# Performance work log

Measured on AMD Instinct MI355X. Metric: run time of the kernel, lower is better.

Reference implementation:

```python
import jax, jax.numpy as jnp
from jax import lax
import numpy as np

HEADS = 4
BUCKET = 64
DEPTH = 4


def _conv(x, w, b):
    y = lax.conv_general_dilated(x, w, (1, 1), [(1, 1), (1, 1)],
                                 dimension_numbers=('NCHW', 'OIHW', 'NCHW'))
    return y + b[None, :, None, None]


def _convT(x, w, b):
    # torch ConvTranspose2d(k=4, s=2, p=1): flip kernel, swap io, lhs_dilation=2, pad k-1-p=2
    wk = jnp.flip(w, (2, 3)).transpose(1, 0, 2, 3)
    y = lax.conv_general_dilated(x, wk, (1, 1), [(2, 2), (2, 2)], lhs_dilation=(2, 2),
                                 dimension_numbers=('NCHW', 'OIHW', 'NCHW'))
    return y + b[None, :, None, None]


def _maxpool(x):
    return lax.reduce_window(x, -jnp.inf, lax.max, (1, 1, 2, 2), (1, 1, 2, 2), 'VALID')


def _ln(x, g, b):
    m = x.mean(-1, keepdims=True)
    v = ((x - m) ** 2).mean(-1, keepdims=True)
    return (x - m) / jnp.sqrt(v + 1e-5) * g + b


def _lsh_attention(x, Wqk, bqk, Wv, bv, Wo, bo, rot):
    # shared-QK LSH bucketed attention (single hash round), look-one-back chunks
    B, N, D = x.shape
    h, dh = HEADS, D // HEADS
    qk = (x @ Wqk + bqk).reshape(B, N, h, dh).transpose(0, 2, 1, 3)  # B h N dh
    v = (x @ Wv + bv).reshape(B, N, h, dh).transpose(0, 2, 1, 3)
    k = qk / (jnp.linalg.norm(qk, axis=-1, keepdims=True) + 1e-6)    # keys = normalized queries
    rotated = jnp.einsum('bhnd,hdr->bhnr', qk, rot)
    buckets = jnp.argmax(jnp.concatenate([rotated, -rotated], -1), -1)  # B h N
    ticker = jnp.arange(N)
    perm = jnp.argsort(buckets * N + ticker, axis=-1)  # stable sort by bucket
    inv_perm = jnp.argsort(perm, axis=-1)
    g = lambda t: jnp.take_along_axis(t, perm[..., None], axis=2)
    nc = N // BUCKET
    bq = g(qk).reshape(B, h, nc, BUCKET, dh)
    bk = g(k).reshape(B, h, nc, BUCKET, dh)
    bv_ = g(v).reshape(B, h, nc, BUCKET, dh)
    bk2 = jnp.concatenate([bk, jnp.roll(bk, 1, axis=2)], axis=3)   # look one chunk back
    bv2 = jnp.concatenate([bv_, jnp.roll(bv_, 1, axis=2)], axis=3)
    dots = jnp.einsum('bhcid,bhcjd->bhcij', bq, bk2) * (dh ** -0.5)
    spos = jnp.take_along_axis(jnp.broadcast_to(ticker, buckets.shape), perm, -1).reshape(B, h, nc, BUCKET)
    kpos = jnp.concatenate([spos, jnp.roll(spos, 1, axis=2)], axis=3)
    dots = jnp.where(spos[..., :, None] == kpos[..., None, :], -1e5, dots)  # mask self (q == k)
    attn = jax.nn.softmax(dots, -1)
    o = jnp.einsum('bhcij,bhcjd->bhcid', attn, bv2).reshape(B, h, N, dh)
    o = jnp.take_along_axis(o, inv_perm[..., None], axis=2)  # unsort
    return o.transpose(0, 2, 1, 3).reshape(B, N, D) @ Wo + bo


def _reformer(seq, ln1_g, ln1_b, Wqk, bqk, Wv, bv, Wo, bo, rot, ln2_g, ln2_b, Wff1, bff1, Wff2, bff2):
    for i in range(DEPTH):
        seq = seq + _lsh_attention(_ln(seq, ln1_g[i], ln1_b[i]), Wqk[i], bqk[i], Wv[i], bv[i], Wo[i], bo[i], rot[i])
        hdn = jax.nn.gelu(_ln(seq, ln2_g[i], ln2_b[i]) @ Wff1[i] + bff1[i])
        seq = seq + hdn @ Wff2[i] + bff2[i]
    return seq


def _forward(burst, conv1_w, conv1_b, conv2_w, conv2_b, conv3_w, conv3_b,
             ln1_g, ln1_b, Wqk, bqk, Wv, bv, Wo, bo, rot, ln2_g, ln2_b,
             Wff1, bff1, Wff2, bff2, up1_w, up1_b, dec1_w, dec1_b,
             up2_w, up2_b, dec2_w, dec2_b, out_w, out_b):
    B, T, C, H, W = burst.shape
    x = burst.reshape(B * T, C, H, W)
    e1 = jax.nn.relu(_conv(x, conv1_w, conv1_b))
    p1 = _maxpool(e1)
    e2 = jax.nn.relu(_conv(p1, conv2_w, conv2_b))
    p2 = _maxpool(e2)
    bm = jax.nn.relu(_conv(p2, conv3_w, conv3_b))
    D = bm.shape[1]
    Hq, Wq = H // 4, W // 4
    seq = bm.transpose(0, 2, 3, 1).reshape(B * T, Hq * Wq, D)
    seq = _reformer(seq, ln1_g, ln1_b, Wqk, bqk, Wv, bv, Wo, bo, rot, ln2_g, ln2_b, Wff1, bff1, Wff2, bff2)
    bm = seq.reshape(B * T, Hq, Wq, D).transpose(0, 3, 1, 2)
    d1 = _convT(bm, up1_w, up1_b)
    d1 = jax.nn.relu(_conv(jnp.concatenate([d1, e2], 1), dec1_w, dec1_b))
    d2 = _convT(d1, up2_w, up2_b)
    d2 = jax.nn.relu(_conv(jnp.concatenate([d2, e1], 1), dec2_w, dec2_b))
    sharp = jax.nn.sigmoid(_conv(d2, out_w, out_b))
    return sharp.reshape(B, T, C, H, W)[:, 0]


def setup_inputs() -> dict:
    key = jax.random.key(0)
    ks = jax.random.split(key, 20)
    s = 0.05
    n = lambda k, shape: jax.random.normal(k, shape, jnp.float32) * s
    inp = {}
    inp['burst'] = jax.random.uniform(ks[0], (1, 7, 3, 256, 256), jnp.float32)
    inp['conv1_w'] = n(ks[1], (64, 3, 3, 3)); inp['conv1_b'] = jnp.zeros((64,), jnp.float32)
    inp['conv2_w'] = n(ks[2], (128, 64, 3, 3)); inp['conv2_b'] = jnp.zeros((128,), jnp.float32)
    inp['conv3_w'] = n(ks[3], (256, 128, 3, 3)); inp['conv3_b'] = jnp.zeros((256,), jnp.float32)
    inp['ln1_g'] = jnp.ones((4, 256), jnp.float32); inp['ln1_b'] = jnp.zeros((4, 256), jnp.float32)
    inp['Wqk'] = n(ks[4], (4, 256, 256)); inp['bqk'] = jnp.zeros((4, 256), jnp.float32)
    inp['Wv'] = n(ks[5], (4, 256, 256)); inp['bv'] = jnp.zeros((4, 256), jnp.float32)
    inp['Wo'] = n(ks[6], (4, 256, 256)); inp['bo'] = jnp.zeros((4, 256), jnp.float32)
    inp['rot'] = jax.random.normal(ks[7], (4, 4, 64, 32), jnp.float32)  # depth, heads, d_head, n_buckets//2
    inp['ln2_g'] = jnp.ones((4, 256), jnp.float32); inp['ln2_b'] = jnp.zeros((4, 256), jnp.float32)
    inp['Wff1'] = n(ks[8], (4, 256, 1024)); inp['bff1'] = jnp.zeros((4, 1024), jnp.float32)
    inp['Wff2'] = n(ks[9], (4, 1024, 256)); inp['bff2'] = jnp.zeros((4, 256), jnp.float32)
    inp['up1_w'] = n(ks[10], (256, 128, 4, 4)); inp['up1_b'] = jnp.zeros((128,), jnp.float32)
    inp['dec1_w'] = n(ks[11], (128, 256, 3, 3)); inp['dec1_b'] = jnp.zeros((128,), jnp.float32)
    inp['up2_w'] = n(ks[12], (128, 64, 4, 4)); inp['up2_b'] = jnp.zeros((64,), jnp.float32)
    inp['dec2_w'] = n(ks[13], (64, 128, 3, 3)); inp['dec2_b'] = jnp.zeros((64,), jnp.float32)
    inp['out_w'] = n(ks[14], (3, 64, 3, 3)); inp['out_b'] = jnp.zeros((3,), jnp.float32)
    return inp


def reference(burst, conv1_w, conv1_b, conv2_w, conv2_b, conv3_w, conv3_b,
              ln1_g, ln1_b, Wqk, bqk, Wv, bv, Wo, bo, rot, ln2_g, ln2_b,
              Wff1, bff1, Wff2, bff2, up1_w, up1_b, dec1_w, dec1_b,
              up2_w, up2_b, dec2_w, dec2_b, out_w, out_b):
    return _forward(burst, conv1_w, conv1_b, conv2_w, conv2_b, conv3_w, conv3_b,
                    ln1_g, ln1_b, Wqk, bqk, Wv, bv, Wo, bo, rot, ln2_g, ln2_b,
                    Wff1, bff1, Wff2, bff2, up1_w, up1_b, dec1_w, dec1_b,
                    up2_w, up2_b, dec2_w, dec2_b, out_w, out_b)
```

## Files before the change

kernel.cpp:

```cpp
#include <hip/hip_runtime.h>
#include <hip/hip_bf16.h>
#include <math.h>

using short8  = __attribute__((ext_vector_type(8))) short;
using half8   = __attribute__((ext_vector_type(8))) _Float16;
using floatx4 = __attribute__((ext_vector_type(4))) float;

static __device__ __forceinline__ float gelu_f(float x) {
    float x3 = x * x * x;
    return 0.5f * x * (1.f + tanhf(0.7978845608028654f * (x + 0.044715f * x3)));
}

static __device__ __forceinline__ short f2h(float f) {
    _Float16 h = (_Float16)f;
    return __builtin_bit_cast(short, h);
}


template <int OCB>
__global__ __launch_bounds__(256) void conv3x3_kernel(
    const float* __restrict__ in1, int C1, const float* __restrict__ in2, int C2,
    const float* __restrict__ w, const float* __restrict__ bias,
    float* __restrict__ out, int H, int W, int OC, int act, int nhwc_out)
{
    int tx = threadIdx.x, ty = threadIdx.y;
    int x = blockIdx.x * 16 + tx, y = blockIdx.y * 16 + ty;
    int oc0 = blockIdx.z * OCB;
    int C = C1 + C2;
    float acc[OCB];
#pragma unroll
    for (int o = 0; o < OCB; ++o) acc[o] = 0.f;
    for (int ic = 0; ic < C; ++ic) {
        const float* src = (ic < C1) ? (in1 + (size_t)ic * H * W)
                                     : (in2 + (size_t)(ic - C1) * H * W);
        float v[9];
#pragma unroll
        for (int ky = 0; ky < 3; ++ky) {
            int iy = y + ky - 1;
            bool okY = (iy >= 0) && (iy < H);
#pragma unroll
            for (int kx = 0; kx < 3; ++kx) {
                int ix = x + kx - 1;
                bool ok = okY && (ix >= 0) && (ix < W);
                v[ky * 3 + kx] = ok ? src[(size_t)iy * W + ix] : 0.f;
            }
        }
        const float* wp = w + ((size_t)oc0 * C + ic) * 9;
#pragma unroll
        for (int o = 0; o < OCB; ++o) {
            const float* wo = wp + (size_t)o * C * 9;
            acc[o] += v[0]*wo[0] + v[1]*wo[1] + v[2]*wo[2]
                    + v[3]*wo[3] + v[4]*wo[4] + v[5]*wo[5]
                    + v[6]*wo[6] + v[7]*wo[7] + v[8]*wo[8];
        }
    }
#pragma unroll
    for (int o = 0; o < OCB; ++o) {
        int oc = oc0 + o;
        float r = acc[o] + bias[oc];
        if (act == 1) r = fmaxf(r, 0.f);
        else if (act == 2) r = 1.f / (1.f + expf(-r));
        if (nhwc_out) out[(size_t)(y * W + x) * OC + oc] = r;
        else          out[(size_t)oc * H * W + (size_t)y * W + x] = r;
    }
}

__global__ __launch_bounds__(256) void conv3x3_lds_kernel(
    const float* __restrict__ in, const float* __restrict__ w,
    const float* __restrict__ bias, float* __restrict__ out,
    int H, int W, int C, int OC, int nhwc_out)
{
    __shared__ float s[16 * 324];
    int tid = threadIdx.x;
    int tx = tid & 15, ty = tid >> 4;
    int x0 = blockIdx.x * 16, y0 = blockIdx.y * 16;
    int oc0 = blockIdx.z * 8;
    int HW = H * W;
    float acc[8];
#pragma unroll
    for (int o = 0; o < 8; ++o) acc[o] = 0.f;
    for (int ic0 = 0; ic0 < C; ic0 += 16) {
        __syncthreads();
        for (int idx = tid; idx < 16 * 324; idx += 256) {
            int ic = idx / 324;
            int r = idx - ic * 324;
            int yy = r / 18;
            int xx = r - yy * 18;
            int gy = y0 + yy - 1, gx = x0 + xx - 1;
            float v = 0.f;
            if (gy >= 0 && gy < H && gx >= 0 && gx < W)
                v = in[(size_t)(ic0 + ic) * HW + (size_t)gy * W + gx];
            s[idx] = v;
        }
        __syncthreads();
        for (int ic = 0; ic < 16; ++ic) {
            const float* sc = s + ic * 324;
            float v[9];
            v[0] = sc[(ty + 0) * 18 + tx + 0];
            v[1] = sc[(ty + 0) * 18 + tx + 1];
            v[2] = sc[(ty + 0) * 18 + tx + 2];
            v[3] = sc[(ty + 1) * 18 + tx + 0];
            v[4] = sc[(ty + 1) * 18 + tx + 1];
            v[5] = sc[(ty + 1) * 18 + tx + 2];
            v[6] = sc[(ty + 2) * 18 + tx + 0];
            v[7] = sc[(ty + 2) * 18 + tx + 1];
            v[8] = sc[(ty + 2) * 18 + tx + 2];
            const float* wp = w + ((size_t)oc0 * C + ic0 + ic) * 9;
#pragma unroll
            for (int o = 0; o < 8; ++o) {
                const float* wo = wp + (size_t)o * C * 9;
                acc[o] += v[0]*wo[0] + v[1]*wo[1] + v[2]*wo[2]
                        + v[3]*wo[3] + v[4]*wo[4] + v[5]*wo[5]
                        + v[6]*wo[6] + v[7]*wo[7] + v[8]*wo[8];
            }
        }
    }
    int x = x0 + tx, y = y0 + ty;
#pragma unroll
    for (int o = 0; o < 8; ++o) {
        int oc = oc0 + o;
        float r = fmaxf(acc[o] + bias[oc], 0.f);
        if (nhwc_out) out[(size_t)(y * W + x) * OC + oc] = r;
        else          out[(size_t)oc * HW + (size_t)y * W + x] = r;
    }
}

__global__ __launch_bounds__(256) void maxpool_kernel(
    const float* __restrict__ in, float* __restrict__ out, int C, int IH, int IW)
{
    int OH = IH >> 1, OW = IW >> 1;
    int idx = blockIdx.x * 256 + threadIdx.x;
    int total = C * OH * OW;
    if (idx >= total) return;
    int x = idx % OW; int t = idx / OW; int y = t % OH; int c = t / OH;
    const float* p = in + (size_t)c * IH * IW + (size_t)(2 * y) * IW + 2 * x;
    out[idx] = fmaxf(fmaxf(p[0], p[1]), fmaxf(p[IW], p[IW + 1]));
}

__global__ __launch_bounds__(256) void ln_kernel(
    const float* __restrict__ x, const float* __restrict__ g,
    const float* __restrict__ b, float* __restrict__ y, short* __restrict__ yh)
{
    int wave = threadIdx.x >> 6, lane = threadIdx.x & 63;
    int n = blockIdx.x * 4 + wave;
    const float* xr = x + (size_t)n * 256;
    float4 v = *(const float4*)(xr + lane * 4);
    float s = v.x + v.y + v.z + v.w;
#pragma unroll
    for (int m = 1; m < 64; m <<= 1) s += __shfl_xor(s, m);
    float mean = s * (1.f / 256.f);
    float cx = v.x - mean, cy = v.y - mean, cz = v.z - mean, cw = v.w - mean;
    float q = cx * cx + cy * cy + cz * cz + cw * cw;
#pragma unroll
    for (int m = 1; m < 64; m <<= 1) q += __shfl_xor(q, m);
    float rstd = rsqrtf(q * (1.f / 256.f) + 1e-5f);
    float4 gv = *(const float4*)(g + lane * 4);
    float4 bv = *(const float4*)(b + lane * 4);
    float4 o;
    o.x = cx * rstd * gv.x + bv.x;
    o.y = cy * rstd * gv.y + bv.y;
    o.z = cz * rstd * gv.z + bv.z;
    o.w = cw * rstd * gv.w + bv.w;
    *(float4*)(y + (size_t)n * 256 + lane * 4) = o;
    short* yp = yh + (size_t)n * 256 + lane * 4;
    yp[0] = f2h(o.x); yp[1] = f2h(o.y); yp[2] = f2h(o.z); yp[3] = f2h(o.w);
}

static __device__ __forceinline__ void gemm_core(
    const float* __restrict__ A, const float* __restrict__ W,
    const float* __restrict__ bias, float* __restrict__ Cp,
    int N, int K, int act, int resid, int m0, int n0)
{
    __shared__ float As[16][68];
    __shared__ float Ws[16][68];
    int tid = threadIdx.x;
    int tx = tid & 15, ty = tid >> 4;
    int lm = tid & 63, lk = (tid >> 6) * 4;
    int lwk = tid >> 4, lwn = (tid & 15) * 4;
    const float* Ap = A + (size_t)(m0 + lm) * K + lk;
    const float* Wp = W + (size_t)lwk * N + n0 + lwn;
    float4 av = *(const float4*)Ap;
    float4 wv = *(const float4*)Wp;
    float acc[4][4];
#pragma unroll
    for (int i = 0; i < 4; ++i)
#pragma unroll
        for (int j = 0; j < 4; ++j) acc[i][j] = 0.f;
    for (int k0 = 0; k0 < K; k0 += 16) {
        As[lk + 0][lm] = av.x; As[lk + 1][lm] = av.y;
        As[lk + 2][lm] = av.z; As[lk + 3][lm] = av.w;
        *(float4*)(&Ws[lwk][lwn]) = wv;
        __syncthreads();
        if (k0 + 16 < K) {
            av = *(const float4*)(Ap + k0 + 16);
            wv = *(const float4*)(Wp + (size_t)(k0 + 16) * N);
        }
#pragma unroll
        for (int kk = 0; kk < 16; ++kk) {
            float4 a4 = *(const float4*)(&As[kk][ty * 4]);
            float4 w4 = *(const float4*)(&Ws[kk][tx * 4]);
            acc[0][0] += a4.x * w4.x; acc[0][1] += a4.x * w4.y; acc[0][2] += a4.x * w4.z; acc[0][3] += a4.x * w4.w;
            acc[1][0] += a4.y * w4.x; acc[1][1] += a4.y * w4.y; acc[1][2] += a4.y * w4.z; acc[1][3] += a4.y * w4.w;
            acc[2][0] += a4.z * w4.x; acc[2][1] += a4.z * w4.y; acc[2][2] += a4.z * w4.z; acc[2][3] += a4.z * w4.w;
            acc[3][0] += a4.w * w4.x; acc[3][1] += a4.w * w4.y; acc[3][2] += a4.w * w4.z; acc[3][3] += a4.w * w4.w;
        }
        __syncthreads();
    }
#pragma unroll
    for (int i = 0; i < 4; ++i) {
        int cm = m0 + ty * 4 + i;
#pragma unroll
        for (int j = 0; j < 4; ++j) {
            int cn = n0 + tx * 4 + j;
            float v = acc[i][j] + bias[cn];
            if (act == 1) v = gelu_f(v);
            float* cp = Cp + (size_t)cm * N + cn;
            if (resid) v += *cp;
            *cp = v;
        }
    }
}

__global__ __launch_bounds__(256) void gemm_kernel(
    const float* __restrict__ A, const float* __restrict__ W,
    const float* __restrict__ bias, float* __restrict__ C,
    int M, int N, int K, int act, int resid)
{
    gemm_core(A, W, bias, C, N, K, act, resid, blockIdx.y * 64, blockIdx.x * 64);
}

__global__ __launch_bounds__(256) void gemm_qkv_kernel(
    const float* __restrict__ A,
    const float* __restrict__ W1, const float* __restrict__ b1, float* __restrict__ C1,
    const float* __restrict__ W2, const float* __restrict__ b2, float* __restrict__ C2,
    int K)
{
    int side = blockIdx.x >> 2;
    const float* W = side ? W2 : W1;
    const float* b = side ? b2 : b1;
    float* C = side ? C2 : C1;
    gemm_core(A, W, b, C, 256, K, 0, 0, blockIdx.y * 64, (blockIdx.x & 3) * 64);
}

__global__ __launch_bounds__(256) void knorm_kernel(
    const float* __restrict__ qk, float* __restrict__ knrm)
{
    int t = blockIdx.x * 256 + threadIdx.x;
    int h = t >> 12, n = t & 4095;
    const float* q = qk + (size_t)n * 256 + h * 64;
    float s = 0.f;
#pragma unroll
    for (int d = 0; d < 64; d += 4) {
        float4 v = *(const float4*)(q + d);
        s += v.x * v.x + v.y * v.y + v.z * v.z + v.w * v.w;
    }
    knrm[t] = 1.f / (sqrtf(s) + 1e-6f);
}

__global__ __launch_bounds__(256) void bucket_kernel(
    const float* __restrict__ qk, const float* __restrict__ rot,
    int* __restrict__ buckets)
{
    int t = blockIdx.x * 256 + threadIdx.x;
    int h = t >> 12, n = t & 4095;
    const float* q = qk + (size_t)n * 256 + h * 64;
    const float* R = rot + (size_t)h * 2048;
    float acc[32];
#pragma unroll
    for (int r = 0; r < 32; ++r) acc[r] = 0.f;
    for (int d = 0; d < 64; ++d) {
        float qd = q[d];
        const float* Rd = R + d * 32;
#pragma unroll
        for (int r = 0; r < 32; ++r) acc[r] += qd * Rd[r];
    }
    float bvv = acc[0]; int best = 0;
#pragma unroll
    for (int j = 1; j < 64; ++j) {
        float val = (j < 32) ? acc[j] : -acc[j - 32];
        if (val > bvv) { bvv = val; best = j; }
    }
    buckets[t] = best;
}

__global__ __launch_bounds__(256) void lsh_sort_kernel(
    const int* __restrict__ buckets, int* __restrict__ perm)
{
    int h = blockIdx.x;
    const int* bk = buckets + h * 4096;
    __shared__ unsigned long long mask[64][64];
    __shared__ int counts[64];
    __shared__ int offsets[64];
    __shared__ int wpre[64][64];
    int tid = threadIdx.x, wave = tid >> 6, lane = tid & 63;
    for (int w = wave * 16; w < wave * 16 + 16; ++w) {
        int bl = bk[w * 64 + lane];
        for (int b = 0; b < 64; ++b) {
            unsigned long long m = __ballot(bl == b);
            if (lane == b) mask[b][w] = m;
        }
    }
    __syncthreads();
    if (tid < 64) {
        int c = 0;
        for (int w = 0; w < 64; ++w) c += __popcll(mask[tid][w]);
        counts[tid] = c;
    }
    __syncthreads();
    if (tid == 0) {
        int a = 0;
        for (int b = 0; b < 64; ++b) { offsets[b] = a; a += counts[b]; }
    }
    __syncthreads();
    for (int b = wave * 16; b < wave * 16 + 16; ++b) {
        int c = __popcll(mask[b][lane]);
        int incl = c;
#pragma unroll
        for (int off = 1; off < 64; off <<= 1) {
            int nb = __shfl_up(incl, off);
            if (lane >= off) incl += nb;
        }
        wpre[b][lane] = incl - c + offsets[b];
    }
    __syncthreads();
    for (int i = tid; i < 4096; i += 256) {
        int b = bk[i]; int w = i >> 6; int l = i & 63;
        unsigned long long below = mask[b][w] & ((1ull << l) - 1ull);
        int pos = wpre[b][w] + __popcll(below);
        perm[h * 4096 + pos] = i;
    }
}

__global__ __launch_bounds__(256) void attn_kernel(
    const float* __restrict__ qk, const float* __restrict__ vv,
    const float* __restrict__ knrm, const int* __restrict__ perm,
    float* __restrict__ o, short* __restrict__ oh)
{
    __shared__ float ks[128 * 64];
    __shared__ float dotsT[128 * 64];
    int c = blockIdx.x, h = blockIdx.y;
    int tid = threadIdx.x;
    const int* pm = perm + h * 4096;
    int cm = (c + 63) & 63;
    {
        int jr = tid >> 1, hf = tid & 1;
        int sk = (jr < 64) ? (c * 64 + jr) : (cm * 64 + (jr - 64));
        int nk = pm[sk];
        float sc = knrm[h * 4096 + nk];
        const float* src = qk + (size_t)nk * 256 + h * 64 + hf * 32;
        float* dst = ks + jr * 64 + hf * 32;
#pragma unroll
        for (int d = 0; d < 32; d += 4) {
            float4 v = *(const float4*)(src + d);
            v.x *= sc; v.y *= sc; v.z *= sc; v.w *= sc;
            *(float4*)(dst + d) = v;
        }
    }
    __syncthreads();
    int r = tid & 63, jg = tid >> 6;
    int nq = pm[c * 64 + r];
    {
        float qreg[64];
        const float* src = qk + (size_t)nq * 256 + h * 64;
#pragma unroll
        for (int d = 0; d < 64; d += 4) {
            float4 v = *(const float4*)(src + d);
            qreg[d] = v.x; qreg[d + 1] = v.y; qreg[d + 2] = v.z; qreg[d + 3] = v.w;
        }
        for (int j = jg * 32; j < jg * 32 + 32; ++j) {
            const float* kr = ks + j * 64;
            float dot = 0.f;
#pragma unroll
            for (int d = 0; d < 64; ++d) dot += qreg[d] * kr[d];
            int sk = (j < 64) ? (c * 64 + j) : (cm * 64 + (j - 64));
            int nk = pm[sk];
            dot = (nk == nq) ? -1e5f : dot * 0.125f;
            dotsT[j * 64 + r] = dot;
        }
    }
    __syncthreads();
    {
        int jr = tid >> 1, hf = tid & 1;
        int sk = (jr < 64) ? (c * 64 + jr) : (cm * 64 + (jr - 64));
        int nk = pm[sk];
        const float* src = vv + (size_t)nk * 256 + h * 64 + hf * 32;
        float* dst = ks + jr * 64 + hf * 32;
#pragma unroll
        for (int d = 0; d < 32; d += 4)
            *(float4*)(dst + d) = *(const float4*)(src + d);
    }
    if (tid < 64) {
        int rr = tid;
        float mx = -1e30f;
        for (int j = 0; j < 128; ++j) mx = fmaxf(mx, dotsT[j * 64 + rr]);
        float s = 0.f;
        for (int j = 0; j < 128; ++j) {
            float e = expf(dotsT[j * 64 + rr] - mx);
            dotsT[j * 64 + rr] = e; s += e;
        }
        float inv = 1.f / s;
        for (int j = 0; j < 128; ++j) dotsT[j * 64 + rr] *= inv;
    }
    __syncthreads();
    int dg = jg;
    float acc[16];
#pragma unroll
    for (int d = 0; d < 16; ++d) acc[d] = 0.f;
    for (int j = 0; j < 128; ++j) {
        float a = dotsT[j * 64 + r];
        const float* vr = ks + j * 64 + dg * 16;
#pragma unroll
        for (int d = 0; d < 16; ++d) acc[d] += a * vr[d];
    }
    size_t ob = (size_t)nq * 256 + h * 64 + dg * 16;
    float* dst = o + ob;
    short* dsth = oh + ob;
#pragma unroll
    for (int d = 0; d < 16; d += 4) {
        float4 v = { acc[d], acc[d + 1], acc[d + 2], acc[d + 3] };
        *(float4*)(dst + d) = v;
        dsth[d] = f2h(v.x); dsth[d+1] = f2h(v.y);
        dsth[d+2] = f2h(v.z); dsth[d+3] = f2h(v.w);
    }
}


__global__ void pack_gemm_kernel(const float* __restrict__ W, short* __restrict__ Bp,
                                 int N, int total)
{
    int t = blockIdx.x * 256 + threadIdx.x;
    if (t >= total) return;
    int lane = t & 63, fi = t >> 6;
    int NT = N >> 4;
    int nt = fi % NT, kt = fi / NT;
    int n = nt * 16 + (lane & 15);
    int k0 = kt * 32 + (lane >> 4) * 8;
    short8 v;
#pragma unroll
    for (int j = 0; j < 8; ++j) v[j] = f2h(W[(size_t)(k0 + j) * N + n]);
    ((short8*)Bp)[t] = v;
}

__global__ void pack_conv_kernel(const float* __restrict__ w, short* __restrict__ Bp,
                                 int C, int OC, int NT, int total)
{
    int t = blockIdx.x * 256 + threadIdx.x;
    if (t >= total) return;
    int lane = t & 63, fi = t >> 6;
    int nt = fi % NT, kt = fi / NT;
    int cpt = C >> 5;
    int tap = kt / cpt, ct = kt % cpt;
    int c = ct * 32 + (lane >> 4) * 8;
    int oc = nt * 16 + (lane & 15);
    short8 v;
#pragma unroll
    for (int j = 0; j < 8; ++j) {
        float f = (oc < OC) ? w[((size_t)oc * C + c + j) * 9 + tap] : 0.f;
        v[j] = f2h(f);
    }
    ((short8*)Bp)[t] = v;
}

__global__ void pack_convt_kernel(const float* __restrict__ w, short* __restrict__ Bp,
                                  int IC, int OC, int total)
{
    int t = blockIdx.x * 256 + threadIdx.x;
    if (t >= total) return;
    int lane = t & 63, fi = t >> 6;
    int NT = OC >> 4, cpt = IC >> 5, KT4 = 4 * cpt;
    int nt = fi % NT, r = fi / NT;
    int kt = r % KT4, pz = r / KT4;
    int py = pz >> 1, px = pz & 1;
    int t4 = kt / cpt, ct = kt % cpt;
    int ty = t4 >> 1, tx = t4 & 1;
    int ky = py ? (2 * ty) : (1 + 2 * ty);
    int kx = px ? (2 * tx) : (1 + 2 * tx);
    int ic = ct * 32 + (lane >> 4) * 8;
    int oc = nt * 16 + (lane & 15);
    short8 v;
#pragma unroll
    for (int j = 0; j < 8; ++j)
        v[j] = f2h(w[(((size_t)(ic + j) * OC + oc) * 4 + ky) * 4 + kx]);
    ((short8*)Bp)[t] = v;
}

__global__ __launch_bounds__(256) void gemm_mfma_kernel(
    const short* __restrict__ A, const short* __restrict__ Bp,
    const float* __restrict__ bias, float* __restrict__ Cf, short* __restrict__ Cb,
    int M, int N, int K, int act, int resid)
{
    int tid = threadIdx.x, wave = tid >> 6, lane = tid & 63;
    int quad = lane >> 4, l16 = lane & 15;
    int m0 = blockIdx.y * 64 + wave * 16;
    int NT = N >> 4;
    int nt0 = blockIdx.x * 4;
    const half8* arow = (const half8*)(A + (size_t)(m0 + l16) * K + quad * 8);
    const half8* bp = (const half8*)Bp;
    floatx4 acc0 = {0,0,0,0}, acc1 = {0,0,0,0}, acc2 = {0,0,0,0}, acc3 = {0,0,0,0};
    int KT = K >> 5;
    for (int kt = 0; kt < KT; ++kt) {
        half8 a = arow[kt * 4];
        size_t bi = ((size_t)kt * NT + nt0) * 64 + lane;
        acc0 = __builtin_amdgcn_mfma_f32_16x16x32_f16(a, bp[bi      ], acc0, 0, 0, 0);
        acc1 = __builtin_amdgcn_mfma_f32_16x16x32_f16(a, bp[bi +  64], acc1, 0, 0, 0);
        acc2 = __builtin_amdgcn_mfma_f32_16x16x32_f16(a, bp[bi + 128], acc2, 0, 0, 0);
        acc3 = __builtin_amdgcn_mfma_f32_16x16x32_f16(a, bp[bi + 192], acc3, 0, 0, 0);
    }
    floatx4 accs[4] = {acc0, acc1, acc2, acc3};
#pragma unroll
    for (int s = 0; s < 4; ++s) {
        int n = (nt0 + s) * 16 + l16;
        float bs = bias[n];
#pragma unroll
        for (int r = 0; r < 4; ++r) {
            int m = m0 + quad * 4 + r;
            float v = accs[s][r] + bs;
            if (act == 1) v = gelu_f(v);
            size_t o = (size_t)m * N + n;
            if (resid) v += Cf[o];
            if (Cb) Cb[o] = f2h(v);
            else    Cf[o] = v;
        }
    }
}

__global__ __launch_bounds__(256) void conv_mfma_kernel(
    const short* __restrict__ in1, int C1, const short* __restrict__ in2, int C2,
    const short* __restrict__ Bp, const float* __restrict__ bias,
    float* __restrict__ outf, short* __restrict__ outb, int H, int W, int OC)
{
    int tid = threadIdx.x, wave = tid >> 6, lane = tid & 63;
    int quad = lane >> 4, l16 = lane & 15;
    int x0 = blockIdx.x * 64, y = blockIdx.y, nt0 = blockIdx.z * 4;
    int C = C1 + C2, cpt = C >> 5, NT = OC >> 4;
    const half8* bp = (const half8*)Bp;
    floatx4 acc0 = {0,0,0,0}, acc1 = {0,0,0,0}, acc2 = {0,0,0,0}, acc3 = {0,0,0,0};
    int xm = x0 + wave * 16 + l16;
    for (int ky = 0; ky < 3; ++ky) {
        int yy = y + ky - 1;
        bool rok = (yy >= 0) && (yy < H);
        for (int kx = 0; kx < 3; ++kx) {
            int xx = xm + kx - 1;
            bool ok = rok && (xx >= 0) && (xx < W);
            int pos = yy * W + xx;
            int ktb = (ky * 3 + kx) * cpt;
            for (int ct = 0; ct < cpt; ++ct) {
                int cc = ct * 32 + quad * 8;
                half8 a = {};
                if (ok) {
                    const short* src = (cc < C1) ? (in1 + (size_t)pos * C1 + cc)
                                                 : (in2 + (size_t)pos * C2 + (cc - C1));
                    a = *(const half8*)src;
                }
                size_t bi = ((size_t)(ktb + ct) * NT + nt0) * 64 + lane;
                acc0 = __builtin_amdgcn_mfma_f32_16x16x32_f16(a, bp[bi      ], acc0, 0, 0, 0);
                acc1 = __builtin_amdgcn_mfma_f32_16x16x32_f16(a, bp[bi +  64], acc1, 0, 0, 0);
                acc2 = __builtin_amdgcn_mfma_f32_16x16x32_f16(a, bp[bi + 128], acc2, 0, 0, 0);
                acc3 = __builtin_amdgcn_mfma_f32_16x16x32_f16(a, bp[bi + 192], acc3, 0, 0, 0);
            }
        }
    }
    floatx4 accs[4] = {acc0, acc1, acc2, acc3};
#pragma unroll
    for (int s = 0; s < 4; ++s) {
        int n = (nt0 + s) * 16 + l16;
        float bs = bias[n];
#pragma unroll
        for (int r = 0; r < 4; ++r) {
            int m = wave * 16 + quad * 4 + r;
            int x = x0 + m;
            float v = fmaxf(accs[s][r] + bs, 0.f);
            size_t o = ((size_t)y * W + x) * OC + n;
            if (outb) outb[o] = f2h(v);
            else      outf[o] = v;
        }
    }
}

__global__ __launch_bounds__(256) void convt_mfma_kernel(
    const short* __restrict__ in, int IC, const short* __restrict__ Bp,
    const float* __restrict__ bias, short* __restrict__ outb, int IH, int IW, int OC)
{
    int tid = threadIdx.x, wave = tid >> 6, lane = tid & 63;
    int quad = lane >> 4, l16 = lane & 15;
    int pz = blockIdx.z & 3, nt0 = (blockIdx.z >> 2) * 4;
    int py = pz >> 1, px = pz & 1;
    int a0 = blockIdx.y, b0 = blockIdx.x * 64;
    int cpt = IC >> 5, NT = OC >> 4, KT4 = 4 * cpt;
    const half8* bp = (const half8*)Bp;
    floatx4 acc0 = {0,0,0,0}, acc1 = {0,0,0,0}, acc2 = {0,0,0,0}, acc3 = {0,0,0,0};
    int bm = b0 + wave * 16 + l16;
    for (int ty = 0; ty < 2; ++ty) {
        int iy = a0 + (py ? (1 - ty) : (-ty));
        bool rok = (iy >= 0) && (iy < IH);
        for (int tx = 0; tx < 2; ++tx) {
            int ix = bm + (px ? (1 - tx) : (-tx));
            bool ok = rok && (ix >= 0) && (ix < IW);
            int pos = iy * IW + ix;
            int ktb = (ty * 2 + tx) * cpt;
            for (int ct = 0; ct < cpt; ++ct) {
                int cc = ct * 32 + quad * 8;
                half8 a = {};
                if (ok) a = *(const half8*)(in + (size_t)pos * IC + cc);
                size_t bi = ((size_t)(pz * KT4 + ktb + ct) * NT + nt0) * 64 + lane;
                acc0 = __builtin_amdgcn_mfma_f32_16x16x32_f16(a, bp[bi      ], acc0, 0, 0, 0);
                acc1 = __builtin_amdgcn_mfma_f32_16x16x32_f16(a, bp[bi +  64], acc1, 0, 0, 0);
                acc2 = __builtin_amdgcn_mfma_f32_16x16x32_f16(a, bp[bi + 128], acc2, 0, 0, 0);
                acc3 = __builtin_amdgcn_mfma_f32_16x16x32_f16(a, bp[bi + 192], acc3, 0, 0, 0);
            }
        }
    }
    floatx4 accs[4] = {acc0, acc1, acc2, acc3};
    int OW = IW * 2;
    int oy = 2 * a0 + py;
#pragma unroll
    for (int s = 0; s < 4; ++s) {
        int n = (nt0 + s) * 16 + l16;
        float bs = bias[n];
#pragma unroll
        for (int r = 0; r < 4; ++r) {
            int m = wave * 16 + quad * 4 + r;
            int ox = 2 * (b0 + m) + px;
            float v = accs[s][r] + bs;
            outb[((size_t)oy * OW + ox) * OC + n] = f2h(v);
        }
    }
}

__global__ __launch_bounds__(256) void convout_mfma_kernel(
    const short* __restrict__ in, const short* __restrict__ Bp,
    const float* __restrict__ bias, float* __restrict__ out, int H, int W)
{
    int tid = threadIdx.x, wave = tid >> 6, lane = tid & 63;
    int quad = lane >> 4, l16 = lane & 15;
    int x0 = blockIdx.x * 64, y = blockIdx.y;
    const int C = 64, cpt = 2;
    const half8* bp = (const half8*)Bp;
    floatx4 acc = {0,0,0,0};
    int xm = x0 + wave * 16 + l16;
    for (int ky = 0; ky < 3; ++ky) {
        int yy = y + ky - 1;
        bool rok = (yy >= 0) && (yy < H);
        for (int kx = 0; kx < 3; ++kx) {
            int xx = xm + kx - 1;
            bool ok = rok && (xx >= 0) && (xx < W);
            int pos = yy * W + xx;
            int ktb = (ky * 3 + kx) * cpt;
#pragma unroll
            for (int ct = 0; ct < cpt; ++ct) {
                int cc = ct * 32 + quad * 8;
                half8 a = {};
                if (ok) a = *(const half8*)(in + (size_t)pos * C + cc);
                acc = __builtin_amdgcn_mfma_f32_16x16x32_f16(
                          a, bp[(size_t)(ktb + ct) * 64 + lane], acc, 0, 0, 0);
            }
        }
    }
    int oc = l16;
    if (oc < 3) {
        float bs = bias[oc];
#pragma unroll
        for (int r = 0; r < 4; ++r) {
            int m = wave * 16 + quad * 4 + r;
            int x = x0 + m;
            float v = acc[r] + bs;
            v = 1.f / (1.f + expf(-v));
            out[(size_t)oc * H * W + (size_t)y * W + x] = v;
        }
    }
}

__global__ __launch_bounds__(256) void nchw2nhwc_h_kernel(
    const float* __restrict__ in, short* __restrict__ out, int C, int HW)
{
    __shared__ float t[32][33];
    int c0 = blockIdx.y * 32, p0 = blockIdx.x * 32;
    int tid = threadIdx.x;
#pragma unroll
    for (int it = 0; it < 4; ++it) {
        int i = tid + it * 256;
        int lc = i >> 5, lp = i & 31;
        t[lc][lp] = in[(size_t)(c0 + lc) * HW + p0 + lp];
    }
    __syncthreads();
#pragma unroll
    for (int it = 0; it < 4; ++it) {
        int i = tid + it * 256;
        int lp = i >> 5, lc = i & 31;
        out[(size_t)(p0 + lp) * C + c0 + lc] = f2h(t[lc][lp]);
    }
}

__global__ __launch_bounds__(256) void f2h_kernel(
    const float* __restrict__ in, short* __restrict__ out, int n)
{
    int i = blockIdx.x * 256 + threadIdx.x;
    if (i < n) out[i] = f2h(in[i]);
}

extern "C" void kernel_launch(void* const* d_in, const int* in_sizes, int n_in,
                              void* d_out, int out_size, void* d_ws, size_t ws_size,
                              hipStream_t stream)
{
    const float* burst   = (const float*)d_in[0];
    const float* conv1_w = (const float*)d_in[1];  const float* conv1_b = (const float*)d_in[2];
    const float* conv2_w = (const float*)d_in[3];  const float* conv2_b = (const float*)d_in[4];
    const float* conv3_w = (const float*)d_in[5];  const float* conv3_b = (const float*)d_in[6];
    const float* ln1_g   = (const float*)d_in[7];  const float* ln1_b   = (const float*)d_in[8];
    const float* Wqk     = (const float*)d_in[9];  const float* bqk     = (const float*)d_in[10];
    const float* Wv      = (const float*)d_in[11]; const float* bvv     = (const float*)d_in[12];
    const float* Wo      = (const float*)d_in[13]; const float* bo      = (const float*)d_in[14];
    const float* rot     = (const float*)d_in[15];
    const float* ln2_g   = (const float*)d_in[16]; const float* ln2_b   = (const float*)d_in[17];
    const float* Wff1    = (const float*)d_in[18]; const float* bff1    = (const float*)d_in[19];
    const float* Wff2    = (const float*)d_in[20]; const float* bff2    = (const float*)d_in[21];
    const float* up1_w   = (const float*)d_in[22]; const float* up1_b   = (const float*)d_in[23];
    const float* dec1_w  = (const float*)d_in[24]; const float* dec1_b  = (const float*)d_in[25];
    const float* up2_w   = (const float*)d_in[26]; const float* up2_b   = (const float*)d_in[27];
    const float* dec2_w  = (const float*)d_in[28]; const float* dec2_b  = (const float*)d_in[29];
    const float* out_w   = (const float*)d_in[30]; const float* out_b   = (const float*)d_in[31];

    float* ws = (float*)d_ws;
    float* e1   = ws + 0;
    float* e2   = ws + 4194304;
    float* p1   = ws + 6291456;
    float* p2   = ws + 7340032;
    float* seq  = ws + 7864320;
    float* xn   = ws + 8912896;
    float* qkb  = ws + 9961472;
    float* vvb  = ws + 11010048;
    float* oob  = ws + 12058624;
    float* hdn  = ws + 13107200;
    float* knb  = ws + 17301504;
    int* buckets = (int*)(ws + 17317888);
    int* perm    = (int*)(ws + 17334272);
    short* xnh  = (short*)p1;
    short* seqh = (short*)(ws + 6815744);
    short* ooh  = (short*)p2;
    short* hdnh = (short*)hdn;
    short* e1h  = (short*)(ws + 15204352);
    short* e2h  = (short*)vvb;
    short* d1   = (short*)xn;
    short* d1c  = (short*)qkb;
    short* d2   = (short*)hdn;
    short* d2c  = (short*)e2;
    short* pk    = (short*)(ws + 17350656);
    short* ppo   = pk + 65536;
    short* ppf1  = pk + 131072;
    short* ppf2  = pk + 393216;
    short* pdec1 = pk + 655360;
    short* pdec2 = pk + 950272;
    short* pout  = pk + 1024000;
    short* pup1  = pk + 1033216;
    short* pup2  = pk + 1557504;

    dim3 b16(16, 16);

    pack_gemm_kernel<<<32, 256, 0, stream>>>(Wo  + 3 * 65536,  ppo,  256, 8192);
    pack_gemm_kernel<<<128, 256, 0, stream>>>(Wff1 + 3 * 262144, ppf1, 1024, 32768);
    pack_gemm_kernel<<<128, 256, 0, stream>>>(Wff2 + 3 * 262144, ppf2, 256, 32768);
    pack_conv_kernel<<<144, 256, 0, stream>>>(dec1_w, pdec1, 256, 128, 8, 36864);
    pack_conv_kernel<<<36, 256, 0, stream>>>(dec2_w, pdec2, 128, 64, 4, 9216);
    pack_conv_kernel<<<5, 256, 0, stream>>>(out_w,  pout,  64, 3, 1, 1152);
    pack_convt_kernel<<<256, 256, 0, stream>>>(up1_w, pup1, 256, 128, 65536);
    pack_convt_kernel<<<64, 256, 0, stream>>>(up2_w, pup2, 128, 64, 16384);

    conv3x3_kernel<8><<<dim3(16, 16, 8), b16, 0, stream>>>(
        burst, 3, nullptr, 0, conv1_w, conv1_b, e1, 256, 256, 64, 1, 0);
    maxpool_kernel<<<4096, 256, 0, stream>>>(e1, p1, 64, 256, 256);
    conv3x3_lds_kernel<<<dim3(8, 8, 16), 256, 0, stream>>>(
        p1, conv2_w, conv2_b, e2, 128, 128, 64, 128, 0);
    maxpool_kernel<<<2048, 256, 0, stream>>>(e2, p2, 128, 128, 128);
    conv3x3_lds_kernel<<<dim3(4, 4, 32), 256, 0, stream>>>(
        p2, conv3_w, conv3_b, seq, 64, 64, 128, 256, 1);

    for (int i = 0; i < 3; ++i) {
        ln_kernel<<<1024, 256, 0, stream>>>(seq, ln1_g + i * 256, ln1_b + i * 256, xn, xnh);
        gemm_qkv_kernel<<<dim3(8, 64), 256, 0, stream>>>(
            xn, Wqk + i * 65536, bqk + i * 256, qkb,
            Wv + i * 65536, bvv + i * 256, vvb, 256);
        knorm_kernel<<<64, 256, 0, stream>>>(qkb, knb);
        bucket_kernel<<<64, 256, 0, stream>>>(qkb, rot + i * 8192, buckets);
        lsh_sort_kernel<<<4, 256, 0, stream>>>(buckets, perm);
        attn_kernel<<<dim3(64, 4), 256, 0, stream>>>(qkb, vvb, knb, perm, oob, ooh);
        gemm_kernel<<<dim3(4, 64), 256, 0, stream>>>(oob, Wo + i * 65536, bo + i * 256,
                                                     seq, 4096, 256, 256, 0, 1);
        ln_kernel<<<1024, 256, 0, stream>>>(seq, ln2_g + i * 256, ln2_b + i * 256, xn, xnh);
        gemm_kernel<<<dim3(16, 64), 256, 0, stream>>>(xn, Wff1 + i * 262144, bff1 + i * 1024,
                                                      hdn, 4096, 1024, 256, 1, 0);
        gemm_kernel<<<dim3(4, 64), 256, 0, stream>>>(hdn, Wff2 + i * 262144, bff2 + i * 256,
                                                     seq, 4096, 256, 1024, 0, 1);
    }

    {
        const int i = 3;
        ln_kernel<<<1024, 256, 0, stream>>>(seq, ln1_g + i * 256, ln1_b + i * 256, xn, xnh);
        gemm_qkv_kernel<<<dim3(8, 64), 256, 0, stream>>>(
            xn, Wqk + i * 65536, bqk + i * 256, qkb,
            Wv + i * 65536, bvv + i * 256, vvb, 256);
        knorm_kernel<<<64, 256, 0, stream>>>(qkb, knb);
        bucket_kernel<<<64, 256, 0, stream>>>(qkb, rot + i * 8192, buckets);
        lsh_sort_kernel<<<4, 256, 0, stream>>>(buckets, perm);
        attn_kernel<<<dim3(64, 4), 256, 0, stream>>>(qkb, vvb, knb, perm, oob, ooh);
        gemm_mfma_kernel<<<dim3(4, 64), 256, 0, stream>>>(
            ooh, ppo, bo + i * 256, seq, nullptr, 4096, 256, 256, 0, 1);
        ln_kernel<<<1024, 256, 0, stream>>>(seq, ln2_g + i * 256, ln2_b + i * 256, xn, xnh);
        gemm_mfma_kernel<<<dim3(16, 64), 256, 0, stream>>>(
            xnh, ppf1, bff1 + i * 1024, nullptr, hdnh, 4096, 1024, 256, 1, 0);
        gemm_mfma_kernel<<<dim3(4, 64), 256, 0, stream>>>(
            hdnh, ppf2, bff2 + i * 256, seq, nullptr, 4096, 256, 1024, 0, 1);
    }

    nchw2nhwc_h_kernel<<<dim3(2048, 2), 256, 0, stream>>>(e1, e1h, 64, 65536);
    nchw2nhwc_h_kernel<<<dim3(512, 4), 256, 0, stream>>>(e2, e2h, 128, 16384);
    f2h_kernel<<<4096, 256, 0, stream>>>(seq, seqh, 1048576);

    convt_mfma_kernel<<<dim3(1, 64, 8), 256, 0, stream>>>(
        seqh, 256, pup1, up1_b, d1, 64, 64, 128);
    conv_mfma_kernel<<<dim3(2, 128, 2), 256, 0, stream>>>(
        d1, 128, e2h, 128, pdec1, dec1_b, nullptr, d1c, 128, 128, 128);
    convt_mfma_kernel<<<dim3(2, 128, 4), 256, 0, stream>>>(
        d1c, 128, pup2, up2_b, d2, 128, 128, 64);
    conv_mfma_kernel<<<dim3(4, 256, 1), 256, 0, stream>>>(
        d2, 64, e1h, 64, pdec2, dec2_b, nullptr, d2c, 256, 256, 64);
    convout_mfma_kernel<<<dim3(4, 256), 256, 0, stream>>>(
        d2c, pout, out_b, (float*)d_out, 256, 256);
}
```

Before: 1.431 ms.

## Run all transformer GEMMs on bf16x3 split-precision MFMA instead of fp32 FMA

Replaces the LDS-tiled fp32 SIMT GEMM used for layers 0-2 (and the fp16 MFMA used for layer 3) with a GEMM that splits each fp32 operand into three bf16 parts and does six MFMA products, giving close to fp32 accuracy on matrix cores. Weights are packed per layer into three bf16 planes by a new packing kernel inside the layer loop, and activations are split on the fly. This removes the scalar-FMA cost of the first three layers, but adds per-layer packing launches and six times the MFMA work per tile. It also removes the fp16 side outputs and dead conv parameters as cleanup.

```diff
diff --git a/kernel.cpp b/kernel.cpp
--- a/kernel.cpp
+++ b/kernel.cpp
@@ -10,29 +10,34 @@
     float x3 = x * x * x;
     return 0.5f * x * (1.f + tanhf(0.7978845608028654f * (x + 0.044715f * x3)));
 }
-
 static __device__ __forceinline__ short f2h(float f) {
     _Float16 h = (_Float16)f;
     return __builtin_bit_cast(short, h);
 }
+static __device__ __forceinline__ short f2bf(float f) {
+    unsigned u = __float_as_uint(f);
+    u += 0x7fffu + ((u >> 16) & 1u);
+    return (short)(u >> 16);
+}
+static __device__ __forceinline__ float bf2f(short s) {
+    return __uint_as_float(((unsigned)(unsigned short)s) << 16);
+}
 
 
 template <int OCB>
 __global__ __launch_bounds__(256) void conv3x3_kernel(
-    const float* __restrict__ in1, int C1, const float* __restrict__ in2, int C2,
+    const float* __restrict__ in1, int C,
     const float* __restrict__ w, const float* __restrict__ bias,
-    float* __restrict__ out, int H, int W, int OC, int act, int nhwc_out)
+    float* __restrict__ out, int H, int W, int OC)
 {
     int tx = threadIdx.x, ty = threadIdx.y;
     int x = blockIdx.x * 16 + tx, y = blockIdx.y * 16 + ty;
     int oc0 = blockIdx.z * OCB;
-    int C = C1 + C2;
     float acc[OCB];
 #pragma unroll
     for (int o = 0; o < OCB; ++o) acc[o] = 0.f;
     for (int ic = 0; ic < C; ++ic) {
-        const float* src = (ic < C1) ? (in1 + (size_t)ic * H * W)
-                                     : (in2 + (size_t)(ic - C1) * H * W);
+        const float* src = in1 + (size_t)ic * H * W;
         float v[9];
 #pragma unroll
         for (int ky = 0; ky < 3; ++ky) {
@@ -57,11 +62,7 @@
 #pragma unroll
     for (int o = 0; o < OCB; ++o) {
         int oc = oc0 + o;
-        float r = acc[o] + bias[oc];
-        if (act == 1) r = fmaxf(r, 0.f);
-        else if (act == 2) r = 1.f / (1.f + expf(-r));
-        if (nhwc_out) out[(size_t)(y * W + x) * OC + oc] = r;
-        else          out[(size_t)oc * H * W + (size_t)y * W + x] = r;
+        out[(size_t)oc * H * W + (size_t)y * W + x] = fmaxf(acc[o] + bias[oc], 0.f);
     }
 }
 
@@ -139,7 +140,7 @@
 
 __global__ __launch_bounds__(256) void ln_kernel(
     const float* __restrict__ x, const float* __restrict__ g,
-    const float* __restrict__ b, float* __restrict__ y, short* __restrict__ yh)
+    const float* __restrict__ b, float* __restrict__ y)
 {
     int wave = threadIdx.x >> 6, lane = threadIdx.x & 63;
     int n = blockIdx.x * 4 + wave;
@@ -162,84 +163,6 @@
     o.z = cz * rstd * gv.z + bv.z;
     o.w = cw * rstd * gv.w + bv.w;
     *(float4*)(y + (size_t)n * 256 + lane * 4) = o;
-    short* yp = yh + (size_t)n * 256 + lane * 4;
-    yp[0] = f2h(o.x); yp[1] = f2h(o.y); yp[2] = f2h(o.z); yp[3] = f2h(o.w);
-}
-
-static __device__ __forceinline__ void gemm_core(
-    const float* __restrict__ A, const float* __restrict__ W,
-    const float* __restrict__ bias, float* __restrict__ Cp,
-    int N, int K, int act, int resid, int m0, int n0)
-{
-    __shared__ float As[16][68];
-    __shared__ float Ws[16][68];
-    int tid = threadIdx.x;
-    int tx = tid & 15, ty = tid >> 4;
-    int lm = tid & 63, lk = (tid >> 6) * 4;
-    int lwk = tid >> 4, lwn = (tid & 15) * 4;
-    const float* Ap = A + (size_t)(m0 + lm) * K + lk;
-    const float* Wp = W + (size_t)lwk * N + n0 + lwn;
-    float4 av = *(const float4*)Ap;
-    float4 wv = *(const float4*)Wp;
-    float acc[4][4];
-#pragma unroll
-    for (int i = 0; i < 4; ++i)
-#pragma unroll
-        for (int j = 0; j < 4; ++j) acc[i][j] = 0.f;
-    for (int k0 = 0; k0 < K; k0 += 16) {
-        As[lk + 0][lm] = av.x; As[lk + 1][lm] = av.y;
-        As[lk + 2][lm] = av.z; As[lk + 3][lm] = av.w;
-        *(float4*)(&Ws[lwk][lwn]) = wv;
-        __syncthreads();
-        if (k0 + 16 < K) {
-            av = *(const float4*)(Ap + k0 + 16);
-            wv = *(const float4*)(Wp + (size_t)(k0 + 16) * N);
-        }
-#pragma unroll
-        for (int kk = 0; kk < 16; ++kk) {
-            float4 a4 = *(const float4*)(&As[kk][ty * 4]);
-            float4 w4 = *(const float4*)(&Ws[kk][tx * 4]);
-            acc[0][0] += a4.x * w4.x; acc[0][1] += a4.x * w4.y; acc[0][2] += a4.x * w4.z; acc[0][3] += a4.x * w4.w;
-            acc[1][0] += a4.y * w4.x; acc[1][1] += a4.y * w4.y; acc[1][2] += a4.y * w4.z; acc[1][3] += a4.y * w4.w;
-            acc[2][0] += a4.z * w4.x; acc[2][1] += a4.z * w4.y; acc[2][2] += a4.z * w4.z; acc[2][3] += a4.z * w4.w;
-            acc[3][0] += a4.w * w4.x; acc[3][1] += a4.w * w4.y; acc[3][2] += a4.w * w4.z; acc[3][3] += a4.w * w4.w;
-        }
-        __syncthreads();
-    }
-#pragma unroll
-    for (int i = 0; i < 4; ++i) {
-        int cm = m0 + ty * 4 + i;
-#pragma unroll
-        for (int j = 0; j < 4; ++j) {
-            int cn = n0 + tx * 4 + j;
-            float v = acc[i][j] + bias[cn];
-            if (act == 1) v = gelu_f(v);
-            float* cp = Cp + (size_t)cm * N + cn;
-            if (resid) v += *cp;
-            *cp = v;
-        }
-    }
-}
-
-__global__ __launch_bounds__(256) void gemm_kernel(
-    const float* __restrict__ A, const float* __restrict__ W,
-    const float* __restrict__ bias, float* __restrict__ C,
-    int M, int N, int K, int act, int resid)
-{
-    gemm_core(A, W, bias, C, N, K, act, resid, blockIdx.y * 64, blockIdx.x * 64);
-}
-
-__global__ __launch_bounds__(256) void gemm_qkv_kernel(
-    const float* __restrict__ A,
-    const float* __restrict__ W1, const float* __restrict__ b1, float* __restrict__ C1,
-    const float* __restrict__ W2, const float* __restrict__ b2, float* __restrict__ C2,
-    int K)
-{
-    int side = blockIdx.x >> 2;
-    const float* W = side ? W2 : W1;
-    const float* b = side ? b2 : b1;
-    float* C = side ? C2 : C1;
-    gemm_core(A, W, b, C, 256, K, 0, 0, blockIdx.y * 64, (blockIdx.x & 3) * 64);
 }
 
 __global__ __launch_bounds__(256) void knorm_kernel(
@@ -334,7 +257,7 @@
 __global__ __launch_bounds__(256) void attn_kernel(
     const float* __restrict__ qk, const float* __restrict__ vv,
     const float* __restrict__ knrm, const int* __restrict__ perm,
-    float* __restrict__ o, short* __restrict__ oh)
+    float* __restrict__ o)
 {
     __shared__ float ks[128 * 64];
     __shared__ float dotsT[128 * 64];
@@ -412,21 +335,18 @@
 #pragma unroll
         for (int d = 0; d < 16; ++d) acc[d] += a * vr[d];
     }
-    size_t ob = (size_t)nq * 256 + h * 64 + dg * 16;
-    float* dst = o + ob;
-    short* dsth = oh + ob;
+    float* dst = o + (size_t)nq * 256 + h * 64 + dg * 16;
 #pragma unroll
     for (int d = 0; d < 16; d += 4) {
         float4 v = { acc[d], acc[d + 1], acc[d + 2], acc[d + 3] };
         *(float4*)(dst + d) = v;
-        dsth[d] = f2h(v.x); dsth[d+1] = f2h(v.y);
-        dsth[d+2] = f2h(v.z); dsth[d+3] = f2h(v.w);
-    }
-}
-
-
-__global__ void pack_gemm_kernel(const float* __restrict__ W, short* __restrict__ Bp,
-                                 int N, int total)
+    }
+}
+
+
+__global__ void pack_gemm3_kernel(const float* __restrict__ W,
+                                  short* __restrict__ B0, short* __restrict__ B1,
+                                  short* __restrict__ B2, int N, int total)
 {
     int t = blockIdx.x * 256 + threadIdx.x;
     if (t >= total) return;
@@ -435,10 +355,100 @@
     int nt = fi % NT, kt = fi / NT;
     int n = nt * 16 + (lane & 15);
     int k0 = kt * 32 + (lane >> 4) * 8;
-    short8 v;
-#pragma unroll
-    for (int j = 0; j < 8; ++j) v[j] = f2h(W[(size_t)(k0 + j) * N + n]);
-    ((short8*)Bp)[t] = v;
+    short8 v0, v1, v2;
+#pragma unroll
+    for (int j = 0; j < 8; ++j) {
+        float v = W[(size_t)(k0 + j) * N + n];
+        short c0 = f2bf(v); float r = v - bf2f(c0);
+        short c1 = f2bf(r); r -= bf2f(c1);
+        short c2 = f2bf(r);
+        v0[j] = c0; v1[j] = c1; v2[j] = c2;
+    }
+    ((short8*)B0)[t] = v0;
+    ((short8*)B1)[t] = v1;
+    ((short8*)B2)[t] = v2;
+}
+
+static __device__ __forceinline__ void gemm_bf3_core(
+    const float* __restrict__ A,
+    const short* __restrict__ B0, const short* __restrict__ B1,
+    const short* __restrict__ B2, const float* __restrict__ bias,
+    float* __restrict__ C, int N, int K, int act, int resid, int bx, int by)
+{
+    int tid = threadIdx.x, wave = tid >> 6, lane = tid & 63;
+    int quad = lane >> 4, l16 = lane & 15;
+    int m0 = by * 64 + wave * 16;
+    int NT = N >> 4, nt0 = bx * 4;
+    const float* arow = A + (size_t)(m0 + l16) * K + quad * 8;
+    const short8* b0p = (const short8*)B0;
+    const short8* b1p = (const short8*)B1;
+    const short8* b2p = (const short8*)B2;
+    floatx4 aM[4] = {{0,0,0,0},{0,0,0,0},{0,0,0,0},{0,0,0,0}};
+    floatx4 aC[4] = {{0,0,0,0},{0,0,0,0},{0,0,0,0},{0,0,0,0}};
+    int KT = K >> 5;
+    for (int kt = 0; kt < KT; ++kt) {
+        float4 u0 = *(const float4*)(arow + kt * 32);
+        float4 u1 = *(const float4*)(arow + kt * 32 + 4);
+        float vv[8] = {u0.x, u0.y, u0.z, u0.w, u1.x, u1.y, u1.z, u1.w};
+        short8 A0, A1, A2;
+#pragma unroll
+        for (int j = 0; j < 8; ++j) {
+            float v = vv[j];
+            short c0 = f2bf(v); float r = v - bf2f(c0);
+            short c1 = f2bf(r); r -= bf2f(c1);
+            short c2 = f2bf(r);
+            A0[j] = c0; A1[j] = c1; A2[j] = c2;
+        }
+        size_t bi = ((size_t)kt * NT + nt0) * 64 + lane;
+#pragma unroll
+        for (int s = 0; s < 4; ++s) {
+            short8 w0 = b0p[bi + s * 64];
+            short8 w1 = b1p[bi + s * 64];
+            short8 w2 = b2p[bi + s * 64];
+            aM[s] = __builtin_amdgcn_mfma_f32_16x16x32_bf16(A0, w0, aM[s], 0, 0, 0);
+            aC[s] = __builtin_amdgcn_mfma_f32_16x16x32_bf16(A0, w1, aC[s], 0, 0, 0);
+            aC[s] = __builtin_amdgcn_mfma_f32_16x16x32_bf16(A1, w0, aC[s], 0, 0, 0);
+            aC[s] = __builtin_amdgcn_mfma_f32_16x16x32_bf16(A0, w2, aC[s], 0, 0, 0);
+            aC[s] = __builtin_amdgcn_mfma_f32_16x16x32_bf16(A1, w1, aC[s], 0, 0, 0);
+            aC[s] = __builtin_amdgcn_mfma_f32_16x16x32_bf16(A2, w0, aC[s], 0, 0, 0);
+        }
+    }
+#pragma unroll
+    for (int s = 0; s < 4; ++s) {
+        int n = (nt0 + s) * 16 + l16;
+        float bs = bias[n];
+#pragma unroll
+        for (int r = 0; r < 4; ++r) {
+            int m = m0 + quad * 4 + r;
+            float v = aM[s][r] + aC[s][r] + bs;
+            if (act == 1) v = gelu_f(v);
+            size_t o = (size_t)m * N + n;
+            if (resid) v += C[o];
+            C[o] = v;
+        }
+    }
+}
+
+__global__ __launch_bounds__(256) void gemm_bf3_kernel(
+    const float* __restrict__ A,
+    const short* __restrict__ B0, const short* __restrict__ B1,
+    const short* __restrict__ B2, const float* __restrict__ bias,
+    float* __restrict__ C, int N, int K, int act, int resid)
+{
+    gemm_bf3_core(A, B0, B1, B2, bias, C, N, K, act, resid, blockIdx.x, blockIdx.y);
+}
+
+__global__ __launch_bounds__(256) void gemm_qkv_bf3_kernel(
+    const float* __restrict__ A,
+    const short* __restrict__ Q0, const short* __restrict__ Q1, const short* __restrict__ Q2,
+    const float* __restrict__ qb, float* __restrict__ Cq,
+    const short* __restrict__ V0, const short* __restrict__ V1, const short* __restrict__ V2,
+    const float* __restrict__ vb, float* __restrict__ Cv, int K)
+{
+    int side = blockIdx.x >> 2;
+    gemm_bf3_core(A, side ? V0 : Q0, side ? V1 : Q1, side ? V2 : Q2,
+                  side ? vb : qb, side ? Cv : Cq, 256, K, 0, 0,
+                  blockIdx.x & 3, blockIdx.y);
 }
 
 __global__ void pack_conv_kernel(const float* __restrict__ w, short* __restrict__ Bp,
@@ -484,57 +494,17 @@
     ((short8*)Bp)[t] = v;
 }
 
-__global__ __launch_bounds__(256) void gemm_mfma_kernel(
-    const short* __restrict__ A, const short* __restrict__ Bp,
-    const float* __restrict__ bias, float* __restrict__ Cf, short* __restrict__ Cb,
-    int M, int N, int K, int act, int resid)
-{
-    int tid = threadIdx.x, wave = tid >> 6, lane = tid & 63;
-    int quad = lane >> 4, l16 = lane & 15;
-    int m0 = blockIdx.y * 64 + wave * 16;
-    int NT = N >> 4;
-    int nt0 = blockIdx.x * 4;
-    const half8* arow = (const half8*)(A + (size_t)(m0 + l16) * K + quad * 8);
-    const half8* bp = (const half8*)Bp;
-    floatx4 acc0 = {0,0,0,0}, acc1 = {0,0,0,0}, acc2 = {0,0,0,0}, acc3 = {0,0,0,0};
-    int KT = K >> 5;
-    for (int kt = 0; kt < KT; ++kt) {
-        half8 a = arow[kt * 4];
-        size_t bi = ((size_t)kt * NT + nt0) * 64 + lane;
-        acc0 = __builtin_amdgcn_mfma_f32_16x16x32_f16(a, bp[bi      ], acc0, 0, 0, 0);
-        acc1 = __builtin_amdgcn_mfma_f32_16x16x32_f16(a, bp[bi +  64], acc1, 0, 0, 0);
-        acc2 = __builtin_amdgcn_mfma_f32_16x16x32_f16(a, bp[bi + 128], acc2, 0, 0, 0);
-        acc3 = __builtin_amdgcn_mfma_f32_16x16x32_f16(a, bp[bi + 192], acc3, 0, 0, 0);
-    }
-    floatx4 accs[4] = {acc0, acc1, acc2, acc3};
-#pragma unroll
-    for (int s = 0; s < 4; ++s) {
-        int n = (nt0 + s) * 16 + l16;
-        float bs = bias[n];
-#pragma unroll
-        for (int r = 0; r < 4; ++r) {
-            int m = m0 + quad * 4 + r;
-            float v = accs[s][r] + bs;
-            if (act == 1) v = gelu_f(v);
-            size_t o = (size_t)m * N + n;
-            if (resid) v += Cf[o];
-            if (Cb) Cb[o] = f2h(v);
-            else    Cf[o] = v;
-        }
-    }
-}
-
 __global__ __launch_bounds__(256) void conv_mfma_kernel(
     const short* __restrict__ in1, int C1, const short* __restrict__ in2, int C2,
     const short* __restrict__ Bp, const float* __restrict__ bias,
-    float* __restrict__ outf, short* __restrict__ outb, int H, int W, int OC)
+    short* __restrict__ outb, int H, int W, int OC)
 {
     int tid = threadIdx.x, wave = tid >> 6, lane = tid & 63;
     int quad = lane >> 4, l16 = lane & 15;
     int x0 = blockIdx.x * 64, y = blockIdx.y, nt0 = blockIdx.z * 4;
     int C = C1 + C2, cpt = C >> 5, NT = OC >> 4;
     const half8* bp = (const half8*)Bp;
-    floatx4 acc0 = {0,0,0,0}, acc1 = {0,0,0,0}, acc2 = {0,0,0,0}, acc3 = {0,0,0,0};
+    floatx4 acc[4] = {{0,0,0,0},{0,0,0,0},{0,0,0,0},{0,0,0,0}};
     int xm = x0 + wave * 16 + l16;
     for (int ky = 0; ky < 3; ++ky) {
         int yy = y + ky - 1;
@@ -542,25 +512,23 @@
         for (int kx = 0; kx < 3; ++kx) {
             int xx = xm + kx - 1;
             bool ok = rok && (xx >= 0) && (xx < W);
-            int pos = yy * W + xx;
+            size_t pos = (size_t)yy * W + xx;
             int ktb = (ky * 3 + kx) * cpt;
             for (int ct = 0; ct < cpt; ++ct) {
                 int cc = ct * 32 + quad * 8;
                 half8 a = {};
                 if (ok) {
-                    const short* src = (cc < C1) ? (in1 + (size_t)pos * C1 + cc)
-                                                 : (in2 + (size_t)pos * C2 + (cc - C1));
+                    const short* src = (cc < C1) ? (in1 + pos * C1 + cc)
+                                                 : (in2 + pos * C2 + (cc - C1));
                     a = *(const half8*)src;
                 }
                 size_t bi = ((size_t)(ktb + ct) * NT + nt0) * 64 + lane;
-                acc0 = __builtin_amdgcn_mfma_f32_16x16x32_f16(a, bp[bi      ], acc0, 0, 0, 0);
-                acc1 = __builtin_amdgcn_mfma_f32_16x16x32_f16(a, bp[bi +  64], acc1, 0, 0, 0);
-                acc2 = __builtin_amdgcn_mfma_f32_16x16x32_f16(a, bp[bi + 128], acc2, 0, 0, 0);
-                acc3 = __builtin_amdgcn_mfma_f32_16x16x32_f16(a, bp[bi + 192], acc3, 0, 0, 0);
+#pragma unroll
+                for (int s = 0; s < 4; ++s)
+                    acc[s] = __builtin_amdgcn_mfma_f32_16x16x32_f16(a, bp[bi + s * 64], acc[s], 0, 0, 0);
             }
         }
     }
-    floatx4 accs[4] = {acc0, acc1, acc2, acc3};
 #pragma unroll
     for (int s = 0; s < 4; ++s) {
         int n = (nt0 + s) * 16 + l16;
@@ -569,10 +537,8 @@
         for (int r = 0; r < 4; ++r) {
             int m = wave * 16 + quad * 4 + r;
             int x = x0 + m;
-            float v = fmaxf(accs[s][r] + bs, 0.f);
-            size_t o = ((size_t)y * W + x) * OC + n;
-            if (outb) outb[o] = f2h(v);
-            else      outf[o] = v;
+            float v = fmaxf(acc[s][r] + bs, 0.f);
+            outb[((size_t)y * W + x) * OC + n] = f2h(v);
         }
     }
 }
@@ -588,7 +554,7 @@
     int a0 = blockIdx.y, b0 = blockIdx.x * 64;
     int cpt = IC >> 5, NT = OC >> 4, KT4 = 4 * cpt;
     const half8* bp = (const half8*)Bp;
-    floatx4 acc0 = {0,0,0,0}, acc1 = {0,0,0,0}, acc2 = {0,0,0,0}, acc3 = {0,0,0,0};
+    floatx4 acc[4] = {{0,0,0,0},{0,0,0,0},{0,0,0,0},{0,0,0,0}};
     int bm = b0 + wave * 16 + l16;
     for (int ty = 0; ty < 2; ++ty) {
         int iy = a0 + (py ? (1 - ty) : (-ty));
@@ -596,21 +562,19 @@
         for (int tx = 0; tx < 2; ++tx) {
             int ix = bm + (px ? (1 - tx) : (-tx));
             bool ok = rok && (ix >= 0) && (ix < IW);
-            int pos = iy * IW + ix;
+            size_t pos = (size_t)iy * IW + ix;
             int ktb = (ty * 2 + tx) * cpt;
             for (int ct = 0; ct < cpt; ++ct) {
                 int cc = ct * 32 + quad * 8;
                 half8 a = {};
-                if (ok) a = *(const half8*)(in + (size_t)pos * IC + cc);
+                if (ok) a = *(const half8*)(in + pos * IC + cc);
                 size_t bi = ((size_t)(pz * KT4 + ktb + ct) * NT + nt0) * 64 + lane;
-                acc0 = __builtin_amdgcn_mfma_f32_16x16x32_f16(a, bp[bi      ], acc0, 0, 0, 0);
-                acc1 = __builtin_amdgcn_mfma_f32_16x16x32_f16(a, bp[bi +  64], acc1, 0, 0, 0);
-                acc2 = __builtin_amdgcn_mfma_f32_16x16x32_f16(a, bp[bi + 128], acc2, 0, 0, 0);
-                acc3 = __builtin_amdgcn_mfma_f32_16x16x32_f16(a, bp[bi + 192], acc3, 0, 0, 0);
+#pragma unroll
+                for (int s = 0; s < 4; ++s)
+                    acc[s] = __builtin_amdgcn_mfma_f32_16x16x32_f16(a, bp[bi + s * 64], acc[s], 0, 0, 0);
             }
         }
     }
-    floatx4 accs[4] = {acc0, acc1, acc2, acc3};
     int OW = IW * 2;
     int oy = 2 * a0 + py;
 #pragma unroll
@@ -621,8 +585,7 @@
         for (int r = 0; r < 4; ++r) {
             int m = wave * 16 + quad * 4 + r;
             int ox = 2 * (b0 + m) + px;
-            float v = accs[s][r] + bs;
-            outb[((size_t)oy * OW + ox) * OC + n] = f2h(v);
+            outb[((size_t)oy * OW + ox) * OC + n] = f2h(acc[s][r] + bs);
         }
     }
 }
@@ -644,13 +607,13 @@
         for (int kx = 0; kx < 3; ++kx) {
             int xx = xm + kx - 1;
             bool ok = rok && (xx >= 0) && (xx < W);
-            int pos = yy * W + xx;
+            size_t pos = (size_t)yy * W + xx;
             int ktb = (ky * 3 + kx) * cpt;
 #pragma unroll
             for (int ct = 0; ct < cpt; ++ct) {
                 int cc = ct * 32 + quad * 8;
                 half8 a = {};
-                if (ok) a = *(const half8*)(in + (size_t)pos * C + cc);
+                if (ok) a = *(const half8*)(in + pos * C + cc);
                 acc = __builtin_amdgcn_mfma_f32_16x16x32_f16(
                           a, bp[(size_t)(ktb + ct) * 64 + lane], acc, 0, 0, 0);
             }
@@ -664,8 +627,7 @@
             int m = wave * 16 + quad * 4 + r;
             int x = x0 + m;
             float v = acc[r] + bs;
-            v = 1.f / (1.f + expf(-v));
-            out[(size_t)oc * H * W + (size_t)y * W + x] = v;
+            out[(size_t)oc * H * W + (size_t)y * W + x] = 1.f / (1.f + expf(-v));
         }
     }
 }
@@ -734,10 +696,14 @@
     float* knb  = ws + 17301504;
     int* buckets = (int*)(ws + 17317888);
     int* perm    = (int*)(ws + 17334272);
-    short* xnh  = (short*)p1;
-    short* seqh = (short*)(ws + 6815744);
-    short* ooh  = (short*)p2;
-    short* hdnh = (short*)hdn;
+    short* pkA  = (short*)p1;
+    short* pf1_0 = pkA;            short* pf1_1 = pkA + 262144;  short* pf1_2 = pkA + 524288;
+    short* pf2_0 = pkA + 786432;   short* pf2_1 = pkA + 1048576; short* pf2_2 = pkA + 1310720;
+    short* pqk_0 = pkA + 1572864;  short* pqk_1 = pkA + 1638400; short* pqk_2 = pkA + 1703936;
+    short* pv_0  = pkA + 1769472;  short* pv_1  = pkA + 1835008; short* pv_2  = pkA + 1900544;
+    short* pkB  = (short*)p2;
+    short* po_0 = pkB; short* po_1 = pkB + 65536; short* po_2 = pkB + 131072;
+    short* seqh = (short*)p2;
     short* e1h  = (short*)(ws + 15204352);
     short* e2h  = (short*)vvb;
     short* d1   = (short*)xn;
@@ -745,28 +711,22 @@
     short* d2   = (short*)hdn;
     short* d2c  = (short*)e2;
     short* pk    = (short*)(ws + 17350656);
-    short* ppo   = pk + 65536;
-    short* ppf1  = pk + 131072;
-    short* ppf2  = pk + 393216;
-    short* pdec1 = pk + 655360;
-    short* pdec2 = pk + 950272;
-    short* pout  = pk + 1024000;
-    short* pup1  = pk + 1033216;
-    short* pup2  = pk + 1557504;
+    short* pdec1 = pk;
+    short* pdec2 = pk + 294912;
+    short* pout  = pk + 368640;
+    short* pup1  = pk + 377856;
+    short* pup2  = pk + 902144;
 
     dim3 b16(16, 16);
 
-    pack_gemm_kernel<<<32, 256, 0, stream>>>(Wo  + 3 * 65536,  ppo,  256, 8192);
-    pack_gemm_kernel<<<128, 256, 0, stream>>>(Wff1 + 3 * 262144, ppf1, 1024, 32768);
-    pack_gemm_kernel<<<128, 256, 0, stream>>>(Wff2 + 3 * 262144, ppf2, 256, 32768);
     pack_conv_kernel<<<144, 256, 0, stream>>>(dec1_w, pdec1, 256, 128, 8, 36864);
     pack_conv_kernel<<<36, 256, 0, stream>>>(dec2_w, pdec2, 128, 64, 4, 9216);
-    pack_conv_kernel<<<5, 256, 0, stream>>>(out_w,  pout,  64, 3, 1, 1152);
+    pack_conv_kernel<<<5, 256, 0, stream>>>(out_w, pout, 64, 3, 1, 1152);
     pack_convt_kernel<<<256, 256, 0, stream>>>(up1_w, pup1, 256, 128, 65536);
     pack_convt_kernel<<<64, 256, 0, stream>>>(up2_w, pup2, 128, 64, 16384);
 
     conv3x3_kernel<8><<<dim3(16, 16, 8), b16, 0, stream>>>(
-        burst, 3, nullptr, 0, conv1_w, conv1_b, e1, 256, 256, 64, 1, 0);
+        burst, 3, conv1_w, conv1_b, e1, 256, 256, 64);
     maxpool_kernel<<<4096, 256, 0, stream>>>(e1, p1, 64, 256, 256);
     conv3x3_lds_kernel<<<dim3(8, 8, 16), 256, 0, stream>>>(
         p1, conv2_w, conv2_b, e2, 128, 128, 64, 128, 0);
@@ -774,41 +734,27 @@
     conv3x3_lds_kernel<<<dim3(4, 4, 32), 256, 0, stream>>>(
         p2, conv3_w, conv3_b, seq, 64, 64, 128, 256, 1);
 
-    for (int i = 0; i < 3; ++i) {
-        ln_kernel<<<1024, 256, 0, stream>>>(seq, ln1_g + i * 256, ln1_b + i * 256, xn, xnh);
-        gemm_qkv_kernel<<<dim3(8, 64), 256, 0, stream>>>(
-            xn, Wqk + i * 65536, bqk + i * 256, qkb,
-            Wv + i * 65536, bvv + i * 256, vvb, 256);
+    for (int i = 0; i < 4; ++i) {
+        pack_gemm3_kernel<<<32, 256, 0, stream>>>(Wqk + i * 65536, pqk_0, pqk_1, pqk_2, 256, 8192);
+        pack_gemm3_kernel<<<32, 256, 0, stream>>>(Wv + i * 65536, pv_0, pv_1, pv_2, 256, 8192);
+        pack_gemm3_kernel<<<32, 256, 0, stream>>>(Wo + i * 65536, po_0, po_1, po_2, 256, 8192);
+        pack_gemm3_kernel<<<128, 256, 0, stream>>>(Wff1 + i * 262144, pf1_0, pf1_1, pf1_2, 1024, 32768);
+        pack_gemm3_kernel<<<128, 256, 0, stream>>>(Wff2 + i * 262144, pf2_0, pf2_1, pf2_2, 256, 32768);
+        ln_kernel<<<1024, 256, 0, stream>>>(seq, ln1_g + i * 256, ln1_b + i * 256, xn);
+        gemm_qkv_bf3_kernel<<<dim3(8, 64), 256, 0, stream>>>(
+            xn, pqk_0, pqk_1, pqk_2, bqk + i * 256, qkb,
+            pv_0, pv_1, pv_2, bvv + i * 256, vvb, 256);
         knorm_kernel<<<64, 256, 0, stream>>>(qkb, knb);
         bucket_kernel<<<64, 256, 0, stream>>>(qkb, rot + i * 8192, buckets);
         lsh_sort_kernel<<<4, 256, 0, stream>>>(buckets, perm);
-        attn_kernel<<<dim3(64, 4), 256, 0, stream>>>(qkb, vvb, knb, perm, oob, ooh);
-        gemm_kernel<<<dim3(4, 64), 256, 0, stream>>>(oob, Wo + i * 65536, bo + i * 256,
-                                                     seq, 4096, 256, 256, 0, 1);
-        ln_kernel<<<1024, 256, 0, stream>>>(seq, ln2_g + i * 256, ln2_b + i * 256, xn, xnh);
-        gemm_kernel<<<dim3(16, 64), 256, 0, stream>>>(xn, Wff1 + i * 262144, bff1 + i * 1024,
-                                                      hdn, 4096, 1024, 256, 1, 0);
-        gemm_kernel<<<dim3(4, 64), 256, 0, stream>>>(hdn, Wff2 + i * 262144, bff2 + i * 256,
-                                                     seq, 4096, 256, 1024, 0, 1);
-    }
-
-    {
-        const int i = 3;
-        ln_kernel<<<1024, 256, 0, stream>>>(seq, ln1_g + i * 256, ln1_b + i * 256, xn, xnh);
-        gemm_qkv_kernel<<<dim3(8, 64), 256, 0, stream>>>(
-            xn, Wqk + i * 65536, bqk + i * 256, qkb,
-            Wv + i * 65536, bvv + i * 256, vvb, 256);
-        knorm_kernel<<<64, 256, 0, stream>>>(qkb, knb);
-        bucket_kernel<<<64, 256, 0, stream>>>(qkb, rot + i * 8192, buckets);
-        lsh_sort_kernel<<<4, 256, 0, stream>>>(buckets, perm);
-        attn_kernel<<<dim3(64, 4), 256, 0, stream>>>(qkb, vvb, knb, perm, oob, ooh);
-        gemm_mfma_kernel<<<dim3(4, 64), 256, 0, stream>>>(
-            ooh, ppo, bo + i * 256, seq, nullptr, 4096, 256, 256, 0, 1);
-        ln_kernel<<<1024, 256, 0, stream>>>(seq, ln2_g + i * 256, ln2_b + i * 256, xn, xnh);
-        gemm_mfma_kernel<<<dim3(16, 64), 256, 0, stream>>>(
-            xnh, ppf1, bff1 + i * 1024, nullptr, hdnh, 4096, 1024, 256, 1, 0);
-        gemm_mfma_kernel<<<dim3(4, 64), 256, 0, stream>>>(
-            hdnh, ppf2, bff2 + i * 256, seq, nullptr, 4096, 256, 1024, 0, 1);
+        attn_kernel<<<dim3(64, 4), 256, 0, stream>>>(qkb, vvb, knb, perm, oob);
+        gemm_bf3_kernel<<<dim3(4, 64), 256, 0, stream>>>(
+            oob, po_0, po_1, po_2, bo + i * 256, seq, 256, 256, 0, 1);
+        ln_kernel<<<1024, 256, 0, stream>>>(seq, ln2_g + i * 256, ln2_b + i * 256, xn);
+        gemm_bf3_kernel<<<dim3(16, 64), 256, 0, stream>>>(
+            xn, pf1_0, pf1_1, pf1_2, bff1 + i * 1024, hdn, 1024, 256, 1, 0);
+        gemm_bf3_kernel<<<dim3(4, 64), 256, 0, stream>>>(
+            hdn, pf2_0, pf2_1, pf2_2, bff2 + i * 256, seq, 256, 1024, 0, 1);
     }
 
     nchw2nhwc_h_kernel<<<dim3(2048, 2), 256, 0, stream>>>(e1, e1h, 64, 65536);
@@ -818,11 +764,11 @@
     convt_mfma_kernel<<<dim3(1, 64, 8), 256, 0, stream>>>(
         seqh, 256, pup1, up1_b, d1, 64, 64, 128);
     conv_mfma_kernel<<<dim3(2, 128, 2), 256, 0, stream>>>(
-        d1, 128, e2h, 128, pdec1, dec1_b, nullptr, d1c, 128, 128, 128);
+        d1, 128, e2h, 128, pdec1, dec1_b, d1c, 128, 128, 128);
     convt_mfma_kernel<<<dim3(2, 128, 4), 256, 0, stream>>>(
         d1c, 128, pup2, up2_b, d2, 128, 128, 64);
     conv_mfma_kernel<<<dim3(4, 256, 1), 256, 0, stream>>>(
-        d2, 64, e1h, 64, pdec2, dec2_b, nullptr, d2c, 256, 256, 64);
+        d2, 64, e1h, 64, pdec2, dec2_b, d2c, 256, 256, 64);
     convout_mfma_kernel<<<dim3(4, 256), 256, 0, stream>>>(
         d2c, pout, out_b, (float*)d_out, 256, 256);
 }
```

After: 1.596 ms. +11.5%, slower.
